# Kernel tuning notes

Hardware: AMD Instinct MI355X
Metric: run time of the kernel (lower is better)

## Reference

```python
import jax, jax.numpy as jnp
import numpy as np

B, T = 8, 1024
D = 256          # n_embd
NH = 4           # n_head
MULT = 4         # mlp_internal_dim_multiplier
GRID = 32        # grid_size, T == GRID*GRID
NLAYER = 3
N = D * MULT // NH   # sparse head dim = 256
EPS = 1e-5


def _freqs_2d(h, w, dim, theta=10000.0):
    # matches get_freqs_2d_fixed: returns (h*w, dim//2) complex64
    dim_half = dim // 2
    freqs = 1.0 / theta ** (np.arange(0, dim_half, 2, dtype=np.float32) / dim_half)
    fx = np.outer(np.arange(w, dtype=np.float32), freqs)
    fy = np.outer(np.arange(h, dtype=np.float32), freqs)
    cx = np.exp(1j * fx).astype(np.complex64)          # (w, dim_half/2)
    cy = np.exp(1j * fy).astype(np.complex64)          # (h, dim_half/2)
    gx = np.broadcast_to(cx[None, :, :], (h, w, cx.shape[-1]))
    gy = np.broadcast_to(cy[:, None, :], (h, w, cy.shape[-1]))
    return np.concatenate([gx, gy], axis=-1).reshape(h * w, -1)

FREQS = jnp.asarray(_freqs_2d(GRID, GRID, N))  # (T, N//2) complex64


def _rope(x):
    # x: (B, nh, T, N) real -> complex pairs, rotate, back to real
    xc = x.reshape(*x.shape[:-1], -1, 2)
    xc = jax.lax.complex(xc[..., 0], xc[..., 1])       # (B, nh, T, N/2)
    xr = xc * FREQS[None, None, :, :]
    out = jnp.stack([jnp.real(xr), jnp.imag(xr)], axis=-1)
    return out.reshape(x.shape).astype(x.dtype)


def _ln(x):
    # LayerNorm over last dim, no affine (biased variance, like torch)
    m = jnp.mean(x, axis=-1, keepdims=True)
    v = jnp.var(x, axis=-1, keepdims=True)
    return (x - m) / jnp.sqrt(v + EPS)


def setup_inputs() -> dict:
    key = jax.random.key(0)
    ks = jax.random.split(key, 6)
    std = 0.02
    return {
        "inputs": jax.random.normal(ks[0], (B, T), dtype=jnp.float32),
        "in_w": jax.random.normal(ks[1], (D, 1), dtype=jnp.float32) * std,
        "in_b": jnp.zeros((D,), dtype=jnp.float32),
        "encoder": jax.random.normal(ks[2], (NH, D, N), dtype=jnp.float32) * std,
        "encoder_v": jax.random.normal(ks[3], (NH, D, N), dtype=jnp.float32) * std,
        "decoder": jax.random.normal(ks[4], (NH * N, D), dtype=jnp.float32) * std,
        "out_w": jax.random.normal(ks[5], (1, D), dtype=jnp.float32) * std,
        "out_b": jnp.zeros((1,), dtype=jnp.float32),
    }


def reference(inputs, in_w, in_b, encoder, encoder_v, decoder, out_w, out_b):
    # input projection: (B,T,1) @ (1,D) + b -> (B,T,D)
    x = inputs[..., None] * in_w[None, None, :, 0].swapaxes(-1, -1)  # placeholder
    x = inputs[..., None] @ in_w.T + in_b                            # (B,T,D)
    x = _ln(x)
    scale = 1.0 / jnp.sqrt(jnp.asarray(N, dtype=x.dtype))
    for _ in range(NLAYER):
        # encoder: (B,T,D) x (nh,D,N) -> (B,nh,T,N)
        x_sparse = jax.nn.relu(jnp.einsum('btd,hdn->bhtn', x, encoder))
        QR = _rope(x_sparse)
        KR = _rope(x_sparse)
        scores = jnp.einsum('bhtn,bhsn->bhts', QR, KR) * scale       # (B,nh,T,T)
        attn = jax.nn.softmax(scores, axis=-1)
        yKV = jnp.einsum('bhts,bsd->bhtd', attn, x)                  # V = x, broadcast over heads
        yKV = _ln(yKV)
        y_sparse = jax.nn.relu(jnp.einsum('bhtd,hdn->bhtn', yKV, encoder_v))
        xy_sparse = x_sparse * y_sparse                              # (B,nh,T,N)
        # (B,nh,T,N) -> (B,T,nh*N) @ (nh*N,D) -> (B,T,D)
        yMLP = xy_sparse.transpose(0, 2, 1, 3).reshape(B, T, NH * N) @ decoder
        x = _ln(x + _ln(yMLP))
    logits = x @ out_w.T + out_b                                     # (B,T,1)
    return logits
```

## Files before the change

### kernel.cpp

```cpp
#include <hip/hip_runtime.h>
#include <hip/hip_bf16.h>
#include <math.h>

#define B_ 8
#define T_ 1024
#define D_ 256
#define NH_ 4
#define N_ 256
#define EPS_ 1e-5f

typedef __attribute__((ext_vector_type(8))) short short8_t;
typedef __attribute__((ext_vector_type(4))) float floatx4;

__device__ inline unsigned short f2bf(float f) {
    unsigned u = __builtin_bit_cast(unsigned, f);
    u += 0x7FFFu + ((u >> 16) & 1u);
    return (unsigned short)(u >> 16);
}
__device__ inline float bf2f(unsigned short h) {
    return __builtin_bit_cast(float, (unsigned)h << 16);
}

__device__ inline void gload_lds16(const unsigned short* g, unsigned short* l) {
    __builtin_amdgcn_global_load_lds(
        (const __attribute__((address_space(1))) unsigned int*)g,
        (__attribute__((address_space(3))) unsigned int*)l, 16, 0, 0);
}

__device__ inline float2 block_stats_256(float v, float* red) {
    float s1 = v, s2 = v * v;
    #pragma unroll
    for (int o = 32; o > 0; o >>= 1) { s1 += __shfl_down(s1, o); s2 += __shfl_down(s2, o); }
    int wave = threadIdx.x >> 6, lane = threadIdx.x & 63;
    __syncthreads();
    if (lane == 0) { red[wave] = s1; red[4 + wave] = s2; }
    __syncthreads();
    float S1 = red[0] + red[1] + red[2] + red[3];
    float S2 = red[4] + red[5] + red[6] + red[7];
    float mean = S1 * (1.f / 256.f);
    float var  = S2 * (1.f / 256.f) - mean * mean;
    return make_float2(mean, var);
}

__global__ __launch_bounds__(256) void k_wT(
    const float* __restrict__ in, unsigned short* __restrict__ outh,
    unsigned short* __restrict__ outl, int R, int C)
{
    __shared__ float tile[64][65];
    int c0 = blockIdx.x * 64, r0 = blockIdx.y * 64, h = blockIdx.z;
    in += (size_t)h * R * C;
    for (int i = threadIdx.x; i < 4096; i += 256) {
        int r = i >> 6, c = i & 63;
        tile[r][c] = in[(size_t)(r0 + r) * C + c0 + c];
    }
    __syncthreads();
    for (int i = threadIdx.x; i < 4096; i += 256) {
        int c = i >> 6, r = i & 63;
        float v = tile[r][c];
        unsigned short hb = f2bf(v);
        size_t o = (size_t)(h * C + c0 + c) * R + r0 + r;
        outh[o] = hb;
        outl[o] = f2bf(v - bf2f(hb));
    }
}

__global__ __launch_bounds__(256) void k_input_ln(
    const float* __restrict__ inputs, const float* __restrict__ in_w,
    const float* __restrict__ in_b, float* __restrict__ x,
    unsigned short* __restrict__ xh, unsigned short* __restrict__ xl)
{
    __shared__ float red[8];
    int row = blockIdx.x;
    int d = threadIdx.x;
    float v = inputs[row] * in_w[d] + in_b[d];
    float2 mv = block_stats_256(v, red);
    float o = (v - mv.x) * rsqrtf(mv.y + EPS_);
    size_t idx = (size_t)row * D_ + d;
    x[idx] = o;
    unsigned short hb = f2bf(o);
    xh[idx] = hb;
    xl[idx] = f2bf(o - bf2f(hb));
}

#define PG 40
template<int MODE>
__global__ __launch_bounds__(256, 2) void k_gemm_mfma(
    const unsigned short* __restrict__ Ah, const unsigned short* __restrict__ Al,
    const unsigned short* __restrict__ Wh, const unsigned short* __restrict__ Wl,
    const unsigned short* __restrict__ xsh, const unsigned short* __restrict__ xsl,
    unsigned short* __restrict__ outh, unsigned short* __restrict__ outl,
    float* __restrict__ outf,
    unsigned short* __restrict__ qrh, unsigned short* __restrict__ qrl)
{
    constexpr int K = (MODE == 2) ? 1024 : 256;
    __shared__ unsigned short As_h[128 * PG], As_l[128 * PG];
    __shared__ unsigned short Ws_h[128 * PG], Ws_l[128 * PG];
    int tid = threadIdx.x;
    int w = tid >> 6, lane = tid & 63, quad = lane >> 4, l16 = lane & 15;
    int wm = w >> 1, wn = w & 1;
    int m0 = blockIdx.y * 128, n0x = blockIdx.x * 128;
    size_t a_row0, w_row0, out_row0;
    int col0;
    int koff = 0, kend = K;
    if (MODE == 1) {
        int bh = blockIdx.z;
        a_row0 = (size_t)bh * 1024 + m0;
        w_row0 = (size_t)((bh & 3) * 256 + n0x);
        out_row0 = (size_t)(bh >> 2) * 1024 + m0;
        col0 = (bh & 3) * 256 + n0x;
    } else {
        a_row0 = m0; w_row0 = n0x; out_row0 = m0; col0 = n0x;
        if (MODE == 2) { koff = blockIdx.z * 256; kend = koff + 256; }
    }
    floatx4 acc[4][4];
    #pragma unroll
    for (int mt = 0; mt < 4; mt++)
        #pragma unroll
        for (int nt = 0; nt < 4; nt++)
            acc[mt][nt] = (floatx4){0.f, 0.f, 0.f, 0.f};

    for (int k0 = koff; k0 < kend; k0 += 32) {
        #pragma unroll
        for (int it = 0; it < 2; it++) {
            int fl = tid + it * 256;
            int row = fl >> 2, ch = fl & 3;
            size_t ga = (a_row0 + row) * (size_t)K + k0 + ch * 8;
            size_t gw = (w_row0 + row) * (size_t)K + k0 + ch * 8;
            *(short8_t*)&As_h[row * PG + ch * 8] = *(const short8_t*)(Ah + ga);
            *(short8_t*)&As_l[row * PG + ch * 8] = *(const short8_t*)(Al + ga);
            *(short8_t*)&Ws_h[row * PG + ch * 8] = *(const short8_t*)(Wh + gw);
            *(short8_t*)&Ws_l[row * PG + ch * 8] = *(const short8_t*)(Wl + gw);
        }
        __syncthreads();
        short8_t afh[4], afl[4], bfh[4], bfl[4];
        #pragma unroll
        for (int mt = 0; mt < 4; mt++) {
            afh[mt] = *(const short8_t*)&As_h[(wm * 64 + mt * 16 + l16) * PG + quad * 8];
            afl[mt] = *(const short8_t*)&As_l[(wm * 64 + mt * 16 + l16) * PG + quad * 8];
        }
        #pragma unroll
        for (int nt = 0; nt < 4; nt++) {
            bfh[nt] = *(const short8_t*)&Ws_h[(wn * 64 + nt * 16 + l16) * PG + quad * 8];
            bfl[nt] = *(const short8_t*)&Ws_l[(wn * 64 + nt * 16 + l16) * PG + quad * 8];
        }
        #pragma unroll
        for (int mt = 0; mt < 4; mt++)
            #pragma unroll
            for (int nt = 0; nt < 4; nt++) {
                acc[mt][nt] = __builtin_amdgcn_mfma_f32_16x16x32_bf16(afh[mt], bfh[nt], acc[mt][nt], 0, 0, 0);
                acc[mt][nt] = __builtin_amdgcn_mfma_f32_16x16x32_bf16(afh[mt], bfl[nt], acc[mt][nt], 0, 0, 0);
                acc[mt][nt] = __builtin_amdgcn_mfma_f32_16x16x32_bf16(afl[mt], bfh[nt], acc[mt][nt], 0, 0, 0);
            }
        __syncthreads();
    }

    #pragma unroll
    for (int mt = 0; mt < 4; mt++) {
        #pragma unroll
        for (int r = 0; r < 4; r++) {
            size_t grow = out_row0 + wm * 64 + mt * 16 + quad * 4 + r;
            #pragma unroll
            for (int nt = 0; nt < 4; nt++) {
                int gcol = col0 + wn * 64 + nt * 16 + l16;
                float v = acc[mt][nt][r];
                if (MODE == 0) {
                    v = fmaxf(v, 0.f);
                    size_t o = grow * 1024 + gcol;
                    unsigned short hb = f2bf(v);
                    outh[o] = hb;
                    outl[o] = f2bf(v - bf2f(hb));
                    float vp = __shfl_xor(v, 1);
                    int n = gcol & 255, h = gcol >> 8;
                    int t = (int)(grow & 1023), b = (int)(grow >> 10);
                    int p = n >> 1, j = p & 63;
                    int pos = (p < 64) ? (t & 31) : (t >> 5);
                    float f = __expf((float)j * -0.14391156f);
                    float ang = (float)pos * f;
                    float sn = __sinf(ang), cs = __cosf(ang);
                    float ro = (n & 1) ? (vp * sn + v * cs) : (v * cs - vp * sn);
                    size_t qo = (((size_t)b * NH_ + h) * T_ + t) * N_ + n;
                    unsigned short qb = f2bf(ro);
                    qrh[qo] = qb;
                    qrl[qo] = f2bf(ro - bf2f(qb));
                } else if (MODE == 1) {
                    float y = fmaxf(v, 0.f);
                    size_t o = grow * 1024 + gcol;
                    float xv = bf2f(xsh[o]) + bf2f(xsl[o]);
                    float p = xv * y;
                    unsigned short hb = f2bf(p);
                    outh[o] = hb;
                    outl[o] = f2bf(p - bf2f(hb));
                } else {
                    outf[(size_t)blockIdx.z * 2097152 + grow * 256 + gcol] = v;
                }
            }
        }
    }
}

__global__ __launch_bounds__(256) void k_xT(const float* __restrict__ x,
                                            unsigned short* __restrict__ Vfh,
                                            unsigned short* __restrict__ Vfl)
{
    __shared__ float tile[64][65];
    int t0 = blockIdx.x * 64, d0 = blockIdx.y * 64, b = blockIdx.z;
    const float* src = x + ((size_t)b * T_ + t0) * D_ + d0;
    for (int i = threadIdx.x; i < 1024; i += 256) {
        int r = i >> 4, c = i & 15;
        float4 v = *(const float4*)(src + (size_t)r * D_ + c * 4);
        tile[r][c * 4 + 0] = v.x;
        tile[r][c * 4 + 1] = v.y;
        tile[r][c * 4 + 2] = v.z;
        tile[r][c * 4 + 3] = v.w;
    }
    __syncthreads();
    for (int i = threadIdx.x; i < 1024; i += 256) {
        int d = i >> 4, c = i & 15;
        int tg = t0 + c * 4;
        int jj = tg >> 5, qd = (tg >> 3) & 3, i8 = tg & 7;
        int dg = d0 + d;
        int tn = dg >> 4, s16 = dg & 15;
        size_t o = (((size_t)b * 32 + jj) * 16 + tn) * 512 + (qd * 16 + s16) * 8 + i8;
        float v0 = tile[c * 4 + 0][d], v1 = tile[c * 4 + 1][d];
        float v2 = tile[c * 4 + 2][d], v3 = tile[c * 4 + 3][d];
        ushort4 oh, ol;
        oh.x = f2bf(v0); ol.x = f2bf(v0 - bf2f(oh.x));
        oh.y = f2bf(v1); ol.y = f2bf(v1 - bf2f(oh.y));
        oh.z = f2bf(v2); ol.z = f2bf(v2 - bf2f(oh.z));
        oh.w = f2bf(v3); ol.w = f2bf(v3 - bf2f(oh.w));
        *(ushort4*)(Vfh + o) = oh;
        *(ushort4*)(Vfl + o) = ol;
    }
}

#define PPW 36

__global__ __launch_bounds__(256, 1) void k_attn_mfma(
    const unsigned short* __restrict__ qr_h, const unsigned short* __restrict__ qr_l,
    const unsigned short* __restrict__ Vf_h, const unsigned short* __restrict__ Vf_l,
    unsigned short* __restrict__ ykvh, unsigned short* __restrict__ ykvl)
{
    __shared__ unsigned short K_h[2][16 * 512];
    __shared__ unsigned short K_l[2][16 * 512];
    __shared__ unsigned short V_h[2][16 * 512];
    __shared__ unsigned short V_l[2][16 * 512];
    __shared__ unsigned short P_h[4][16 * PPW];
    __shared__ unsigned short P_l[4][16 * PPW];

    int tid = threadIdx.x;
    int w = tid >> 6, lane = tid & 63, quad = lane >> 4, l16 = lane & 15;
    int gid = blockIdx.x;
    int bh = gid & 31, tile = gid >> 5, b = bh >> 2;
    int t0q = tile * 128;
    const unsigned short* qhb = qr_h + (size_t)bh * T_ * N_;
    const unsigned short* qlb = qr_l + (size_t)bh * T_ * N_;
    const unsigned short* vhb = Vf_h + (size_t)b * 32 * 16 * 512;
    const unsigned short* vlb = Vf_l + (size_t)b * 32 * 16 * 512;

    short8_t qfh[2][8], qfl[2][8];
    #pragma unroll
    for (int mt = 0; mt < 2; mt++)
        #pragma unroll
        for (int kc = 0; kc < 8; kc++) {
            size_t o = (size_t)(t0q + w * 32 + mt * 16 + l16) * N_ + kc * 32 + quad * 8;
            qfh[mt][kc] = *(const short8_t*)(qhb + o);
            qfl[mt][kc] = *(const short8_t*)(qlb + o);
        }

    floatx4 O[2][16];
    #pragma unroll
    for (int mt = 0; mt < 2; mt++)
        #pragma unroll
        for (int tn = 0; tn < 16; tn++) O[mt][tn] = (floatx4){0.f, 0.f, 0.f, 0.f};
    float lst[2][4] = {{0.f, 0.f, 0.f, 0.f}, {0.f, 0.f, 0.f, 0.f}};
    const float scale = 0.0625f;

    #pragma unroll
    for (int s = 0; s < 4; s++) {
        int slot = w * 4 + s;
        int ct = slot >> 3, kc = slot & 7;
        size_t go = (size_t)(ct * 16 + l16) * N_ + kc * 32 + quad * 8;
        gload_lds16(qhb + go, &K_h[0][slot * 512]);
        gload_lds16(qlb + go, &K_l[0][slot * 512]);
        size_t vo = ((size_t)slot << 9) + lane * 8;
        gload_lds16(vhb + vo, &V_h[0][slot * 512]);
        gload_lds16(vlb + vo, &V_l[0][slot * 512]);
    }

    for (int j = 0; j < 32; j++) {
        int buf = j & 1;
        __syncthreads();
        if (j < 31) {
            #pragma unroll
            for (int s = 0; s < 4; s++) {
                int slot = w * 4 + s;
                int ct = slot >> 3, kc = slot & 7;
                size_t go = (size_t)((j + 1) * 32 + ct * 16 + l16) * N_ + kc * 32 + quad * 8;
                gload_lds16(qhb + go, &K_h[buf ^ 1][slot * 512]);
                gload_lds16(qlb + go, &K_l[buf ^ 1][slot * 512]);
                size_t vo = ((size_t)((j + 1) * 16 + slot) << 9) + lane * 8;
                gload_lds16(vhb + vo, &V_h[buf ^ 1][slot * 512]);
                gload_lds16(vlb + vo, &V_l[buf ^ 1][slot * 512]);
            }
        }

        floatx4 sc[2][2];
        __builtin_amdgcn_s_setprio(1);
        #pragma unroll
        for (int ct = 0; ct < 2; ct++) {
            floatx4 a_hh0 = (floatx4){0.f, 0.f, 0.f, 0.f};
            floatx4 a_hl0 = (floatx4){0.f, 0.f, 0.f, 0.f};
            floatx4 a_lh0 = (floatx4){0.f, 0.f, 0.f, 0.f};
            floatx4 a_hh1 = (floatx4){0.f, 0.f, 0.f, 0.f};
            floatx4 a_hl1 = (floatx4){0.f, 0.f, 0.f, 0.f};
            floatx4 a_lh1 = (floatx4){0.f, 0.f, 0.f, 0.f};
            #pragma unroll
            for (int kc = 0; kc < 8; kc++) {
                short8_t bkh = *(const short8_t*)&K_h[buf][(ct * 8 + kc) * 512 + lane * 8];
                short8_t bkl = *(const short8_t*)&K_l[buf][(ct * 8 + kc) * 512 + lane * 8];
                a_hh0 = __builtin_amdgcn_mfma_f32_16x16x32_bf16(qfh[0][kc], bkh, a_hh0, 0, 0, 0);
                a_hh1 = __builtin_amdgcn_mfma_f32_16x16x32_bf16(qfh[1][kc], bkh, a_hh1, 0, 0, 0);
                a_hl0 = __builtin_amdgcn_mfma_f32_16x16x32_bf16(qfh[0][kc], bkl, a_hl0, 0, 0, 0);
                a_hl1 = __builtin_amdgcn_mfma_f32_16x16x32_bf16(qfh[1][kc], bkl, a_hl1, 0, 0, 0);
                a_lh0 = __builtin_amdgcn_mfma_f32_16x16x32_bf16(qfl[0][kc], bkh, a_lh0, 0, 0, 0);
                a_lh1 = __builtin_amdgcn_mfma_f32_16x16x32_bf16(qfl[1][kc], bkh, a_lh1, 0, 0, 0);
            }
            sc[0][ct] = (a_hh0 + a_hl0) + a_lh0;
            sc[1][ct] = (a_hh1 + a_hl1) + a_lh1;
        }
        __builtin_amdgcn_s_setprio(0);

        short8_t pah[2], pal[2];
        #pragma unroll
        for (int mt = 0; mt < 2; mt++) {
            #pragma unroll
            for (int r = 0; r < 4; r++) {
                float p0 = __expf(sc[mt][0][r] * scale - 8.f);
                float p1 = __expf(sc[mt][1][r] * scale - 8.f);
                lst[mt][r] += p0 + p1;
                unsigned short p0h = f2bf(p0), p1h = f2bf(p1);
                P_h[w][(quad * 4 + r) * PPW + l16]      = p0h;
                P_h[w][(quad * 4 + r) * PPW + 16 + l16] = p1h;
                P_l[w][(quad * 4 + r) * PPW + l16]      = f2bf(p0 - bf2f(p0h));
                P_l[w][(quad * 4 + r) * PPW + 16 + l16] = f2bf(p1 - bf2f(p1h));
            }
            pah[mt] = *(const short8_t*)&P_h[w][l16 * PPW + quad * 8];
            pal[mt] = *(const short8_t*)&P_l[w][l16 * PPW + quad * 8];
        }

        __builtin_amdgcn_s_setprio(1);
        #pragma unroll
        for (int tn = 0; tn < 16; tn++) {
            short8_t vbh = *(const short8_t*)&V_h[buf][tn * 512 + lane * 8];
            short8_t vbl = *(const short8_t*)&V_l[buf][tn * 512 + lane * 8];
            O[0][tn] = __builtin_amdgcn_mfma_f32_16x16x32_bf16(pah[0], vbh, O[0][tn], 0, 0, 0);
            O[1][tn] = __builtin_amdgcn_mfma_f32_16x16x32_bf16(pah[1], vbh, O[1][tn], 0, 0, 0);
            O[0][tn] = __builtin_amdgcn_mfma_f32_16x16x32_bf16(pah[0], vbl, O[0][tn], 0, 0, 0);
            O[1][tn] = __builtin_amdgcn_mfma_f32_16x16x32_bf16(pah[1], vbl, O[1][tn], 0, 0, 0);
            O[0][tn] = __builtin_amdgcn_mfma_f32_16x16x32_bf16(pal[0], vbh, O[0][tn], 0, 0, 0);
            O[1][tn] = __builtin_amdgcn_mfma_f32_16x16x32_bf16(pal[1], vbh, O[1][tn], 0, 0, 0);
        }
        __builtin_amdgcn_s_setprio(0);
    }

    #pragma unroll
    for (int mt = 0; mt < 2; mt++) {
        size_t obase = ((size_t)bh * T_ + t0q + w * 32 + mt * 16) * D_;
        #pragma unroll
        for (int r = 0; r < 4; r++) {
            float lsum = lst[mt][r];
            #pragma unroll
            for (int o = 1; o < 16; o <<= 1) lsum += __shfl_xor(lsum, o);
            float li = 1.f / lsum;
            float s1 = 0.f, s2 = 0.f;
            #pragma unroll
            for (int tn = 0; tn < 16; tn++) { float v = O[mt][tn][r]; s1 += v; s2 += v * v; }
            #pragma unroll
            for (int o = 1; o < 16; o <<= 1) { s1 += __shfl_xor(s1, o); s2 += __shfl_xor(s2, o); }
            float mean = s1 * li * (1.f / 256.f);
            float e2   = s2 * li * li * (1.f / 256.f);
            float var  = e2 - mean * mean;
            float rs = rsqrtf(var + EPS_);
            float a = li * rs, bb = mean * rs;
            int row = quad * 4 + r;
            #pragma unroll
            for (int tn = 0; tn < 16; tn++) {
                float v = O[mt][tn][r] * a - bb;
                size_t o = obase + (size_t)row * D_ + tn * 16 + l16;
                unsigned short hb = f2bf(v);
                ykvh[o] = hb;
                ykvl[o] = f2bf(v - bf2f(hb));
            }
        }
    }
}

__global__ __launch_bounds__(256) void k_resid_ln(float* __restrict__ x,
                                                  const float* __restrict__ ymlp,
                                                  unsigned short* __restrict__ xh,
                                                  unsigned short* __restrict__ xl)
{
    __shared__ float red[8];
    int row = blockIdx.x, d = threadIdx.x;
    size_t o = (size_t)row * D_ + d;
    float y = ymlp[o] + ymlp[o + 2097152] + ymlp[o + 2 * 2097152] + ymlp[o + 3 * 2097152];
    float2 mv1 = block_stats_256(y, red);
    float v = x[o] + (y - mv1.x) * rsqrtf(mv1.y + EPS_);
    float2 mv2 = block_stats_256(v, red);
    float out = (v - mv2.x) * rsqrtf(mv2.y + EPS_);
    x[o] = out;
    unsigned short hb = f2bf(out);
    xh[o] = hb;
    xl[o] = f2bf(out - bf2f(hb));
}

__global__ __launch_bounds__(256) void k_logits(
    const float* __restrict__ x, const float* __restrict__ out_w,
    const float* __restrict__ out_b, float* __restrict__ out)
{
    __shared__ float red[4];
    int row = blockIdx.x, d = threadIdx.x;
    float v = x[(size_t)row * D_ + d] * out_w[d];
    #pragma unroll
    for (int o = 32; o > 0; o >>= 1) v += __shfl_down(v, o);
    int wave = d >> 6, lane = d & 63;
    if (lane == 0) red[wave] = v;
    __syncthreads();
    if (d == 0) out[row] = red[0] + red[1] + red[2] + red[3] + out_b[0];
}

extern "C" void kernel_launch(void* const* d_in, const int* in_sizes, int n_in,
                              void* d_out, int out_size, void* d_ws, size_t ws_size,
                              hipStream_t stream)
{
    (void)in_sizes; (void)n_in; (void)out_size;
    if (ws_size < ((size_t)115 << 20)) return;

    const float* inputs    = (const float*)d_in[0];
    const float* in_w      = (const float*)d_in[1];
    const float* in_b      = (const float*)d_in[2];
    const float* encoder   = (const float*)d_in[3];
    const float* encoder_v = (const float*)d_in[4];
    const float* decoder   = (const float*)d_in[5];
    const float* out_w     = (const float*)d_in[6];
    const float* out_b     = (const float*)d_in[7];

    char* wsb = (char*)d_ws;
    float* x             = (float*)(wsb);
    unsigned short* x_h  = (unsigned short*)(wsb + ((size_t)8  << 20));
    unsigned short* x_l  = (unsigned short*)(wsb + ((size_t)12 << 20));
    unsigned short* Vf_h = x_h;
    unsigned short* Vf_l = x_l;
    unsigned short* xs_h = (unsigned short*)(wsb + ((size_t)16 << 20));
    unsigned short* xs_l = (unsigned short*)(wsb + ((size_t)32 << 20));
    float* ymlp          = (float*)(wsb + ((size_t)16 << 20));
    unsigned short* qr_h = (unsigned short*)(wsb + ((size_t)48 << 20));
    unsigned short* qr_l = (unsigned short*)(wsb + ((size_t)64 << 20));
    unsigned short* xy_h = qr_h;
    unsigned short* xy_l = qr_l;
    unsigned short* ykv_h = (unsigned short*)(wsb + ((size_t)80 << 20));
    unsigned short* ykv_l = (unsigned short*)(wsb + ((size_t)96 << 20));
    char* wbase = wsb + ((size_t)112 << 20);
    unsigned short* encT_h = (unsigned short*)(wbase);
    unsigned short* encT_l = (unsigned short*)(wbase + 0x80000);
    unsigned short* evT_h  = (unsigned short*)(wbase + 2 * 0x80000);
    unsigned short* evT_l  = (unsigned short*)(wbase + 3 * 0x80000);
    unsigned short* decT_h = (unsigned short*)(wbase + 4 * 0x80000);
    unsigned short* decT_l = (unsigned short*)(wbase + 5 * 0x80000);

    k_wT<<<dim3(4, 4, 4), 256, 0, stream>>>(encoder,   encT_h, encT_l, 256, 256);
    k_wT<<<dim3(4, 4, 4), 256, 0, stream>>>(encoder_v, evT_h,  evT_l,  256, 256);
    k_wT<<<dim3(4, 16, 1), 256, 0, stream>>>(decoder,  decT_h, decT_l, 1024, 256);

    k_input_ln<<<B_ * T_, 256, 0, stream>>>(inputs, in_w, in_b, x, x_h, x_l);
    for (int l = 0; l < 3; l++) {
        k_gemm_mfma<0><<<dim3(8, 64, 1), 256, 0, stream>>>(
            x_h, x_l, encT_h, encT_l, nullptr, nullptr, xs_h, xs_l, nullptr, qr_h, qr_l);
        k_xT<<<dim3(16, 4, 8), 256, 0, stream>>>(x, Vf_h, Vf_l);
        k_attn_mfma<<<256, 256, 0, stream>>>(qr_h, qr_l, Vf_h, Vf_l, ykv_h, ykv_l);
        k_gemm_mfma<1><<<dim3(2, 8, 32), 256, 0, stream>>>(
            ykv_h, ykv_l, evT_h, evT_l, xs_h, xs_l, xy_h, xy_l, nullptr, nullptr, nullptr);
        k_gemm_mfma<2><<<dim3(2, 64, 4), 256, 0, stream>>>(
            xy_h, xy_l, decT_h, decT_l, nullptr, nullptr, nullptr, nullptr, ymlp, nullptr, nullptr);
        k_resid_ln<<<B_ * T_, 256, 0, stream>>>(x, ymlp, x_h, x_l);
    }
    k_logits<<<B_ * T_, 256, 0, stream>>>(x, out_w, out_b, (float*)d_out);
}
```

Baseline: 827.8 us.

## Split attention key range across two warp groups with LDS reduction

The attention kernel now launches 512 threads per block: two groups of four waves each process half of the key/value sequence (16 chunks each) for the same 128 query rows. The partial outputs and row sums from the second group are then combined through shared memory before the LayerNorm epilogue. Double buffering is replaced by single-buffered per-group K/V tiles, refilled after a barrier once each phase has finished reading them. This doubles the waves per CU to hide latency and shortens the serial loop, at the cost of extra barriers, exposed load latency and a shared-memory reduction.

```diff
diff --git a/kernel.cpp b/kernel.cpp
--- a/kernel.cpp
+++ b/kernel.cpp
@@ -235,7 +235,7 @@
 
 #define PPW 36
 
-__global__ __launch_bounds__(256, 1) void k_attn_mfma(
+__global__ __launch_bounds__(512, 1) void k_attn_mfma(
     const unsigned short* __restrict__ qr_h, const unsigned short* __restrict__ qr_l,
     const unsigned short* __restrict__ Vf_h, const unsigned short* __restrict__ Vf_l,
     unsigned short* __restrict__ ykvh, unsigned short* __restrict__ ykvl)
@@ -244,11 +244,13 @@
     __shared__ unsigned short K_l[2][16 * 512];
     __shared__ unsigned short V_h[2][16 * 512];
     __shared__ unsigned short V_l[2][16 * 512];
-    __shared__ unsigned short P_h[4][16 * PPW];
-    __shared__ unsigned short P_l[4][16 * PPW];
+    __shared__ unsigned short P_h[8][16 * PPW];
+    __shared__ unsigned short P_l[8][16 * PPW];
+    __shared__ float l_scr[4][32];
 
     int tid = threadIdx.x;
     int w = tid >> 6, lane = tid & 63, quad = lane >> 4, l16 = lane & 15;
+    int tm = w >> 2, wp = w & 3;
     int gid = blockIdx.x;
     int bh = gid & 31, tile = gid >> 5, b = bh >> 2;
     int t0q = tile * 128;
@@ -262,7 +264,7 @@
     for (int mt = 0; mt < 2; mt++)
         #pragma unroll
         for (int kc = 0; kc < 8; kc++) {
-            size_t o = (size_t)(t0q + w * 32 + mt * 16 + l16) * N_ + kc * 32 + quad * 8;
+            size_t o = (size_t)(t0q + wp * 32 + mt * 16 + l16) * N_ + kc * 32 + quad * 8;
             qfh[mt][kc] = *(const short8_t*)(qhb + o);
             qfl[mt][kc] = *(const short8_t*)(qlb + o);
         }
@@ -277,33 +279,18 @@
 
     #pragma unroll
     for (int s = 0; s < 4; s++) {
-        int slot = w * 4 + s;
-        int ct = slot >> 3, kc = slot & 7;
-        size_t go = (size_t)(ct * 16 + l16) * N_ + kc * 32 + quad * 8;
-        gload_lds16(qhb + go, &K_h[0][slot * 512]);
-        gload_lds16(qlb + go, &K_l[0][slot * 512]);
-        size_t vo = ((size_t)slot << 9) + lane * 8;
-        gload_lds16(vhb + vo, &V_h[0][slot * 512]);
-        gload_lds16(vlb + vo, &V_l[0][slot * 512]);
-    }
-
-    for (int j = 0; j < 32; j++) {
-        int buf = j & 1;
-        __syncthreads();
-        if (j < 31) {
-            #pragma unroll
-            for (int s = 0; s < 4; s++) {
-                int slot = w * 4 + s;
-                int ct = slot >> 3, kc = slot & 7;
-                size_t go = (size_t)((j + 1) * 32 + ct * 16 + l16) * N_ + kc * 32 + quad * 8;
-                gload_lds16(qhb + go, &K_h[buf ^ 1][slot * 512]);
-                gload_lds16(qlb + go, &K_l[buf ^ 1][slot * 512]);
-                size_t vo = ((size_t)((j + 1) * 16 + slot) << 9) + lane * 8;
-                gload_lds16(vhb + vo, &V_h[buf ^ 1][slot * 512]);
-                gload_lds16(vlb + vo, &V_l[buf ^ 1][slot * 512]);
-            }
-        }
-
+        int s4 = wp * 4 + s;
+        int ct = s4 >> 3, kc = s4 & 7;
+        size_t go = (size_t)(tm * 512 + ct * 16 + l16) * N_ + kc * 32 + quad * 8;
+        gload_lds16(qhb + go, &K_h[tm][s4 * 512]);
+        gload_lds16(qlb + go, &K_l[tm][s4 * 512]);
+        size_t vo = ((size_t)(tm * 256 + s4) << 9) + lane * 8;
+        gload_lds16(vhb + vo, &V_h[tm][s4 * 512]);
+        gload_lds16(vlb + vo, &V_l[tm][s4 * 512]);
+    }
+    __syncthreads();
+
+    for (int j = 0; j < 16; j++) {
         floatx4 sc[2][2];
         __builtin_amdgcn_s_setprio(1);
         #pragma unroll
@@ -316,8 +303,8 @@
             floatx4 a_lh1 = (floatx4){0.f, 0.f, 0.f, 0.f};
             #pragma unroll
             for (int kc = 0; kc < 8; kc++) {
-                short8_t bkh = *(const short8_t*)&K_h[buf][(ct * 8 + kc) * 512 + lane * 8];
-                short8_t bkl = *(const short8_t*)&K_l[buf][(ct * 8 + kc) * 512 + lane * 8];
+                short8_t bkh = *(const short8_t*)&K_h[tm][(ct * 8 + kc) * 512 + lane * 8];
+                short8_t bkl = *(const short8_t*)&K_l[tm][(ct * 8 + kc) * 512 + lane * 8];
                 a_hh0 = __builtin_amdgcn_mfma_f32_16x16x32_bf16(qfh[0][kc], bkh, a_hh0, 0, 0, 0);
                 a_hh1 = __builtin_amdgcn_mfma_f32_16x16x32_bf16(qfh[1][kc], bkh, a_hh1, 0, 0, 0);
                 a_hl0 = __builtin_amdgcn_mfma_f32_16x16x32_bf16(qfh[0][kc], bkl, a_hl0, 0, 0, 0);
@@ -329,6 +316,18 @@
             sc[1][ct] = (a_hh1 + a_hl1) + a_lh1;
         }
         __builtin_amdgcn_s_setprio(0);
+
+        __syncthreads();
+        if (j < 15) {
+            #pragma unroll
+            for (int s = 0; s < 4; s++) {
+                int s4 = wp * 4 + s;
+                int ct = s4 >> 3, kc = s4 & 7;
+                size_t go = (size_t)((tm * 16 + j + 1) * 32 + ct * 16 + l16) * N_ + kc * 32 + quad * 8;
+                gload_lds16(qhb + go, &K_h[tm][s4 * 512]);
+                gload_lds16(qlb + go, &K_l[tm][s4 * 512]);
+            }
+        }
 
         short8_t pah[2], pal[2];
         #pragma unroll
@@ -351,8 +350,8 @@
         __builtin_amdgcn_s_setprio(1);
         #pragma unroll
         for (int tn = 0; tn < 16; tn++) {
-            short8_t vbh = *(const short8_t*)&V_h[buf][tn * 512 + lane * 8];
-            short8_t vbl = *(const short8_t*)&V_l[buf][tn * 512 + lane * 8];
+            short8_t vbh = *(const short8_t*)&V_h[tm][tn * 512 + lane * 8];
+            short8_t vbl = *(const short8_t*)&V_l[tm][tn * 512 + lane * 8];
             O[0][tn] = __builtin_amdgcn_mfma_f32_16x16x32_bf16(pah[0], vbh, O[0][tn], 0, 0, 0);
             O[1][tn] = __builtin_amdgcn_mfma_f32_16x16x32_bf16(pah[1], vbh, O[1][tn], 0, 0, 0);
             O[0][tn] = __builtin_amdgcn_mfma_f32_16x16x32_bf16(pah[0], vbl, O[0][tn], 0, 0, 0);
@@ -361,35 +360,71 @@
             O[1][tn] = __builtin_amdgcn_mfma_f32_16x16x32_bf16(pal[1], vbh, O[1][tn], 0, 0, 0);
         }
         __builtin_amdgcn_s_setprio(0);
-    }
-
-    #pragma unroll
-    for (int mt = 0; mt < 2; mt++) {
-        size_t obase = ((size_t)bh * T_ + t0q + w * 32 + mt * 16) * D_;
-        #pragma unroll
-        for (int r = 0; r < 4; r++) {
-            float lsum = lst[mt][r];
-            #pragma unroll
-            for (int o = 1; o < 16; o <<= 1) lsum += __shfl_xor(lsum, o);
-            float li = 1.f / lsum;
-            float s1 = 0.f, s2 = 0.f;
-            #pragma unroll
-            for (int tn = 0; tn < 16; tn++) { float v = O[mt][tn][r]; s1 += v; s2 += v * v; }
-            #pragma unroll
-            for (int o = 1; o < 16; o <<= 1) { s1 += __shfl_xor(s1, o); s2 += __shfl_xor(s2, o); }
-            float mean = s1 * li * (1.f / 256.f);
-            float e2   = s2 * li * li * (1.f / 256.f);
-            float var  = e2 - mean * mean;
-            float rs = rsqrtf(var + EPS_);
-            float a = li * rs, bb = mean * rs;
-            int row = quad * 4 + r;
-            #pragma unroll
-            for (int tn = 0; tn < 16; tn++) {
-                float v = O[mt][tn][r] * a - bb;
-                size_t o = obase + (size_t)row * D_ + tn * 16 + l16;
-                unsigned short hb = f2bf(v);
-                ykvh[o] = hb;
-                ykvl[o] = f2bf(v - bf2f(hb));
+
+        __syncthreads();
+        if (j < 15) {
+            #pragma unroll
+            for (int s = 0; s < 4; s++) {
+                int s4 = wp * 4 + s;
+                size_t vo = ((size_t)((tm * 16 + j + 1) * 16 + s4) << 9) + lane * 8;
+                gload_lds16(vhb + vo, &V_h[tm][s4 * 512]);
+                gload_lds16(vlb + vo, &V_l[tm][s4 * 512]);
+            }
+        }
+    }
+
+    float* scr = (float*)((wp == 0) ? (void*)K_h : (wp == 1) ? (void*)K_l
+                        : (wp == 2) ? (void*)V_h : (void*)V_l);
+    if (tm == 1) {
+        #pragma unroll
+        for (int mt = 0; mt < 2; mt++)
+            #pragma unroll
+            for (int r = 0; r < 4; r++) {
+                float ls = lst[mt][r];
+                #pragma unroll
+                for (int o = 1; o < 16; o <<= 1) ls += __shfl_xor(ls, o);
+                int row = mt * 16 + quad * 4 + r;
+                if (l16 == 0) l_scr[wp][row] = ls;
+                #pragma unroll
+                for (int tn = 0; tn < 16; tn++)
+                    scr[row * 256 + tn * 16 + l16] = O[mt][tn][r];
+            }
+    }
+    __syncthreads();
+
+    if (tm == 0) {
+        #pragma unroll
+        for (int mt = 0; mt < 2; mt++) {
+            size_t obase = ((size_t)bh * T_ + t0q + wp * 32 + mt * 16) * D_;
+            #pragma unroll
+            for (int r = 0; r < 4; r++) {
+                int row = quad * 4 + r;
+                #pragma unroll
+                for (int tn = 0; tn < 16; tn++)
+                    O[mt][tn][r] += scr[(mt * 16 + row) * 256 + tn * 16 + l16];
+                float lsum = lst[mt][r];
+                #pragma unroll
+                for (int o = 1; o < 16; o <<= 1) lsum += __shfl_xor(lsum, o);
+                lsum += l_scr[wp][mt * 16 + row];
+                float li = 1.f / lsum;
+                float s1 = 0.f, s2 = 0.f;
+                #pragma unroll
+                for (int tn = 0; tn < 16; tn++) { float v = O[mt][tn][r]; s1 += v; s2 += v * v; }
+                #pragma unroll
+                for (int o = 1; o < 16; o <<= 1) { s1 += __shfl_xor(s1, o); s2 += __shfl_xor(s2, o); }
+                float mean = s1 * li * (1.f / 256.f);
+                float e2   = s2 * li * li * (1.f / 256.f);
+                float var  = e2 - mean * mean;
+                float rs = rsqrtf(var + EPS_);
+                float a = li * rs, bb = mean * rs;
+                #pragma unroll
+                for (int tn = 0; tn < 16; tn++) {
+                    float v = O[mt][tn][r] * a - bb;
+                    size_t o = obase + (size_t)row * D_ + tn * 16 + l16;
+                    unsigned short hb = f2bf(v);
+                    ykvh[o] = hb;
+                    ykvl[o] = f2bf(v - bf2f(hb));
+                }
             }
         }
     }
@@ -477,7 +512,7 @@
         k_gemm_mfma<0><<<dim3(8, 64, 1), 256, 0, stream>>>(
             x_h, x_l, encT_h, encT_l, nullptr, nullptr, xs_h, xs_l, nullptr, qr_h, qr_l);
         k_xT<<<dim3(16, 4, 8), 256, 0, stream>>>(x, Vf_h, Vf_l);
-        k_attn_mfma<<<256, 256, 0, stream>>>(qr_h, qr_l, Vf_h, Vf_l, ykv_h, ykv_l);
+        k_attn_mfma<<<256, 512, 0, stream>>>(qr_h, qr_l, Vf_h, Vf_l, ykv_h, ykv_l);
         k_gemm_mfma<1><<<dim3(2, 8, 32), 256, 0, stream>>>(
             ykv_h, ykv_l, evT_h, evT_l, xs_h, xs_l, xy_h, xy_l, nullptr, nullptr, nullptr);
         k_gemm_mfma<2><<<dim3(2, 64, 4), 256, 0, stream>>>(
```

New measurement: 1.774 ms. 2.14x slower.

## Split attention work across wave pairs with 512-thread blocks

Applied to the files above, without the earlier changes.

The attention kernel now runs 8 waves per block instead of 4. Each pair of waves shares a 32-row query group, and each wave handles half of the key columns for the scores and half of the output columns for P·V. The P tile is written to shared memory by both halves, which adds a block barrier in the middle of each iteration; the K prefetch moves after that barrier while the V prefetch stays before it. Row sums and LayerNorm statistics are combined across the pair through shared-memory scratch before normalisation. The aim is more waves per CU to hide latency and fewer accumulator registers per wave, at the cost of an extra __syncthreads per key tile and duplicated Q fragment loads.

```diff
diff --git a/kernel.cpp b/kernel.cpp
--- a/kernel.cpp
+++ b/kernel.cpp
@@ -233,9 +233,9 @@
     }
 }
 
-#define PPW 36
-
-__global__ __launch_bounds__(256, 1) void k_attn_mfma(
+#define PPW2 36
+
+__global__ __launch_bounds__(512, 1) void k_attn_mfma(
     const unsigned short* __restrict__ qr_h, const unsigned short* __restrict__ qr_l,
     const unsigned short* __restrict__ Vf_h, const unsigned short* __restrict__ Vf_l,
     unsigned short* __restrict__ ykvh, unsigned short* __restrict__ ykvl)
@@ -244,11 +244,15 @@
     __shared__ unsigned short K_l[2][16 * 512];
     __shared__ unsigned short V_h[2][16 * 512];
     __shared__ unsigned short V_l[2][16 * 512];
-    __shared__ unsigned short P_h[4][16 * PPW];
-    __shared__ unsigned short P_l[4][16 * PPW];
+    __shared__ unsigned short P_h[4][32 * PPW2];
+    __shared__ unsigned short P_l[4][32 * PPW2];
+    __shared__ float l_scr[8][32];
+    __shared__ float s1_scr[8][32];
+    __shared__ float s2_scr[8][32];
 
     int tid = threadIdx.x;
     int w = tid >> 6, lane = tid & 63, quad = lane >> 4, l16 = lane & 15;
+    int rg = w >> 1, half = w & 1;
     int gid = blockIdx.x;
     int bh = gid & 31, tile = gid >> 5, b = bh >> 2;
     int t0q = tile * 128;
@@ -262,22 +266,22 @@
     for (int mt = 0; mt < 2; mt++)
         #pragma unroll
         for (int kc = 0; kc < 8; kc++) {
-            size_t o = (size_t)(t0q + w * 32 + mt * 16 + l16) * N_ + kc * 32 + quad * 8;
+            size_t o = (size_t)(t0q + rg * 32 + mt * 16 + l16) * N_ + kc * 32 + quad * 8;
             qfh[mt][kc] = *(const short8_t*)(qhb + o);
             qfl[mt][kc] = *(const short8_t*)(qlb + o);
         }
 
-    floatx4 O[2][16];
+    floatx4 O[2][8];
     #pragma unroll
     for (int mt = 0; mt < 2; mt++)
         #pragma unroll
-        for (int tn = 0; tn < 16; tn++) O[mt][tn] = (floatx4){0.f, 0.f, 0.f, 0.f};
+        for (int t = 0; t < 8; t++) O[mt][t] = (floatx4){0.f, 0.f, 0.f, 0.f};
     float lst[2][4] = {{0.f, 0.f, 0.f, 0.f}, {0.f, 0.f, 0.f, 0.f}};
     const float scale = 0.0625f;
 
     #pragma unroll
-    for (int s = 0; s < 4; s++) {
-        int slot = w * 4 + s;
+    for (int s = 0; s < 2; s++) {
+        int slot = w * 2 + s;
         int ct = slot >> 3, kc = slot & 7;
         size_t go = (size_t)(ct * 16 + l16) * N_ + kc * 32 + quad * 8;
         gload_lds16(qhb + go, &K_h[0][slot * 512]);
@@ -292,107 +296,123 @@
         __syncthreads();
         if (j < 31) {
             #pragma unroll
-            for (int s = 0; s < 4; s++) {
-                int slot = w * 4 + s;
+            for (int s = 0; s < 2; s++) {
+                int slot = w * 2 + s;
+                size_t vo = ((size_t)((j + 1) * 16 + slot) << 9) + lane * 8;
+                gload_lds16(vhb + vo, &V_h[buf ^ 1][slot * 512]);
+                gload_lds16(vlb + vo, &V_l[buf ^ 1][slot * 512]);
+            }
+        }
+
+        floatx4 a_hh0 = (floatx4){0.f, 0.f, 0.f, 0.f};
+        floatx4 a_hl0 = (floatx4){0.f, 0.f, 0.f, 0.f};
+        floatx4 a_lh0 = (floatx4){0.f, 0.f, 0.f, 0.f};
+        floatx4 a_hh1 = (floatx4){0.f, 0.f, 0.f, 0.f};
+        floatx4 a_hl1 = (floatx4){0.f, 0.f, 0.f, 0.f};
+        floatx4 a_lh1 = (floatx4){0.f, 0.f, 0.f, 0.f};
+        __builtin_amdgcn_s_setprio(1);
+        #pragma unroll
+        for (int kc = 0; kc < 8; kc++) {
+            short8_t bkh = *(const short8_t*)&K_h[buf][(half * 8 + kc) * 512 + lane * 8];
+            short8_t bkl = *(const short8_t*)&K_l[buf][(half * 8 + kc) * 512 + lane * 8];
+            a_hh0 = __builtin_amdgcn_mfma_f32_16x16x32_bf16(qfh[0][kc], bkh, a_hh0, 0, 0, 0);
+            a_hh1 = __builtin_amdgcn_mfma_f32_16x16x32_bf16(qfh[1][kc], bkh, a_hh1, 0, 0, 0);
+            a_hl0 = __builtin_amdgcn_mfma_f32_16x16x32_bf16(qfh[0][kc], bkl, a_hl0, 0, 0, 0);
+            a_hl1 = __builtin_amdgcn_mfma_f32_16x16x32_bf16(qfh[1][kc], bkl, a_hl1, 0, 0, 0);
+            a_lh0 = __builtin_amdgcn_mfma_f32_16x16x32_bf16(qfl[0][kc], bkh, a_lh0, 0, 0, 0);
+            a_lh1 = __builtin_amdgcn_mfma_f32_16x16x32_bf16(qfl[1][kc], bkh, a_lh1, 0, 0, 0);
+        }
+        __builtin_amdgcn_s_setprio(0);
+        floatx4 sc0 = (a_hh0 + a_hl0) + a_lh0;
+        floatx4 sc1 = (a_hh1 + a_hl1) + a_lh1;
+
+        #pragma unroll
+        for (int r = 0; r < 4; r++) {
+            float p0 = __expf(sc0[r] * scale - 8.f);
+            float p1 = __expf(sc1[r] * scale - 8.f);
+            lst[0][r] += p0;
+            lst[1][r] += p1;
+            int row0 = quad * 4 + r, row1 = 16 + quad * 4 + r;
+            unsigned short p0h = f2bf(p0), p1h = f2bf(p1);
+            P_h[rg][row0 * PPW2 + half * 16 + l16] = p0h;
+            P_h[rg][row1 * PPW2 + half * 16 + l16] = p1h;
+            P_l[rg][row0 * PPW2 + half * 16 + l16] = f2bf(p0 - bf2f(p0h));
+            P_l[rg][row1 * PPW2 + half * 16 + l16] = f2bf(p1 - bf2f(p1h));
+        }
+
+        __syncthreads();
+        if (j < 31) {
+            #pragma unroll
+            for (int s = 0; s < 2; s++) {
+                int slot = w * 2 + s;
                 int ct = slot >> 3, kc = slot & 7;
                 size_t go = (size_t)((j + 1) * 32 + ct * 16 + l16) * N_ + kc * 32 + quad * 8;
                 gload_lds16(qhb + go, &K_h[buf ^ 1][slot * 512]);
                 gload_lds16(qlb + go, &K_l[buf ^ 1][slot * 512]);
-                size_t vo = ((size_t)((j + 1) * 16 + slot) << 9) + lane * 8;
-                gload_lds16(vhb + vo, &V_h[buf ^ 1][slot * 512]);
-                gload_lds16(vlb + vo, &V_l[buf ^ 1][slot * 512]);
             }
         }
 
-        floatx4 sc[2][2];
+        short8_t pah0 = *(const short8_t*)&P_h[rg][(l16) * PPW2 + quad * 8];
+        short8_t pal0 = *(const short8_t*)&P_l[rg][(l16) * PPW2 + quad * 8];
+        short8_t pah1 = *(const short8_t*)&P_h[rg][(16 + l16) * PPW2 + quad * 8];
+        short8_t pal1 = *(const short8_t*)&P_l[rg][(16 + l16) * PPW2 + quad * 8];
+
         __builtin_amdgcn_s_setprio(1);
         #pragma unroll
-        for (int ct = 0; ct < 2; ct++) {
-            floatx4 a_hh0 = (floatx4){0.f, 0.f, 0.f, 0.f};
-            floatx4 a_hl0 = (floatx4){0.f, 0.f, 0.f, 0.f};
-            floatx4 a_lh0 = (floatx4){0.f, 0.f, 0.f, 0.f};
-            floatx4 a_hh1 = (floatx4){0.f, 0.f, 0.f, 0.f};
-            floatx4 a_hl1 = (floatx4){0.f, 0.f, 0.f, 0.f};
-            floatx4 a_lh1 = (floatx4){0.f, 0.f, 0.f, 0.f};
-            #pragma unroll
-            for (int kc = 0; kc < 8; kc++) {
-                short8_t bkh = *(const short8_t*)&K_h[buf][(ct * 8 + kc) * 512 + lane * 8];
-                short8_t bkl = *(const short8_t*)&K_l[buf][(ct * 8 + kc) * 512 + lane * 8];
-                a_hh0 = __builtin_amdgcn_mfma_f32_16x16x32_bf16(qfh[0][kc], bkh, a_hh0, 0, 0, 0);
-                a_hh1 = __builtin_amdgcn_mfma_f32_16x16x32_bf16(qfh[1][kc], bkh, a_hh1, 0, 0, 0);
-                a_hl0 = __builtin_amdgcn_mfma_f32_16x16x32_bf16(qfh[0][kc], bkl, a_hl0, 0, 0, 0);
-                a_hl1 = __builtin_amdgcn_mfma_f32_16x16x32_bf16(qfh[1][kc], bkl, a_hl1, 0, 0, 0);
-                a_lh0 = __builtin_amdgcn_mfma_f32_16x16x32_bf16(qfl[0][kc], bkh, a_lh0, 0, 0, 0);
-                a_lh1 = __builtin_amdgcn_mfma_f32_16x16x32_bf16(qfl[1][kc], bkh, a_lh1, 0, 0, 0);
-            }
-            sc[0][ct] = (a_hh0 + a_hl0) + a_lh0;
-            sc[1][ct] = (a_hh1 + a_hl1) + a_lh1;
-        }
-        __builtin_amdgcn_s_setprio(0);
-
-        short8_t pah[2], pal[2];
-        #pragma unroll
-        for (int mt = 0; mt < 2; mt++) {
-            #pragma unroll
-            for (int r = 0; r < 4; r++) {
-                float p0 = __expf(sc[mt][0][r] * scale - 8.f);
-                float p1 = __expf(sc[mt][1][r] * scale - 8.f);
-                lst[mt][r] += p0 + p1;
-                unsigned short p0h = f2bf(p0), p1h = f2bf(p1);
-                P_h[w][(quad * 4 + r) * PPW + l16]      = p0h;
-                P_h[w][(quad * 4 + r) * PPW + 16 + l16] = p1h;
-                P_l[w][(quad * 4 + r) * PPW + l16]      = f2bf(p0 - bf2f(p0h));
-                P_l[w][(quad * 4 + r) * PPW + 16 + l16] = f2bf(p1 - bf2f(p1h));
-            }
-            pah[mt] = *(const short8_t*)&P_h[w][l16 * PPW + quad * 8];
-            pal[mt] = *(const short8_t*)&P_l[w][l16 * PPW + quad * 8];
-        }
-
-        __builtin_amdgcn_s_setprio(1);
-        #pragma unroll
-        for (int tn = 0; tn < 16; tn++) {
+        for (int t = 0; t < 8; t++) {
+            int tn = half * 8 + t;
             short8_t vbh = *(const short8_t*)&V_h[buf][tn * 512 + lane * 8];
             short8_t vbl = *(const short8_t*)&V_l[buf][tn * 512 + lane * 8];
-            O[0][tn] = __builtin_amdgcn_mfma_f32_16x16x32_bf16(pah[0], vbh, O[0][tn], 0, 0, 0);
-            O[1][tn] = __builtin_amdgcn_mfma_f32_16x16x32_bf16(pah[1], vbh, O[1][tn], 0, 0, 0);
-            O[0][tn] = __builtin_amdgcn_mfma_f32_16x16x32_bf16(pah[0], vbl, O[0][tn], 0, 0, 0);
-            O[1][tn] = __builtin_amdgcn_mfma_f32_16x16x32_bf16(pah[1], vbl, O[1][tn], 0, 0, 0);
-            O[0][tn] = __builtin_amdgcn_mfma_f32_16x16x32_bf16(pal[0], vbh, O[0][tn], 0, 0, 0);
-            O[1][tn] = __builtin_amdgcn_mfma_f32_16x16x32_bf16(pal[1], vbh, O[1][tn], 0, 0, 0);
+            O[0][t] = __builtin_amdgcn_mfma_f32_16x16x32_bf16(pah0, vbh, O[0][t], 0, 0, 0);
+            O[1][t] = __builtin_amdgcn_mfma_f32_16x16x32_bf16(pah1, vbh, O[1][t], 0, 0, 0);
+            O[0][t] = __builtin_amdgcn_mfma_f32_16x16x32_bf16(pah0, vbl, O[0][t], 0, 0, 0);
+            O[1][t] = __builtin_amdgcn_mfma_f32_16x16x32_bf16(pah1, vbl, O[1][t], 0, 0, 0);
+            O[0][t] = __builtin_amdgcn_mfma_f32_16x16x32_bf16(pal0, vbh, O[0][t], 0, 0, 0);
+            O[1][t] = __builtin_amdgcn_mfma_f32_16x16x32_bf16(pal1, vbh, O[1][t], 0, 0, 0);
         }
         __builtin_amdgcn_s_setprio(0);
     }
 
     #pragma unroll
-    for (int mt = 0; mt < 2; mt++) {
-        size_t obase = ((size_t)bh * T_ + t0q + w * 32 + mt * 16) * D_;
+    for (int mt = 0; mt < 2; mt++)
         #pragma unroll
         for (int r = 0; r < 4; r++) {
-            float lsum = lst[mt][r];
-            #pragma unroll
-            for (int o = 1; o < 16; o <<= 1) lsum += __shfl_xor(lsum, o);
-            float li = 1.f / lsum;
+            float ls = lst[mt][r];
+            #pragma unroll
+            for (int o = 1; o < 16; o <<= 1) ls += __shfl_xor(ls, o);
             float s1 = 0.f, s2 = 0.f;
             #pragma unroll
-            for (int tn = 0; tn < 16; tn++) { float v = O[mt][tn][r]; s1 += v; s2 += v * v; }
+            for (int t = 0; t < 8; t++) { float v = O[mt][t][r]; s1 += v; s2 += v * v; }
             #pragma unroll
             for (int o = 1; o < 16; o <<= 1) { s1 += __shfl_xor(s1, o); s2 += __shfl_xor(s2, o); }
+            int row = mt * 16 + quad * 4 + r;
+            if (l16 == 0) { l_scr[w][row] = ls; s1_scr[w][row] = s1; s2_scr[w][row] = s2; }
+        }
+    __syncthreads();
+    #pragma unroll
+    for (int mt = 0; mt < 2; mt++)
+        #pragma unroll
+        for (int r = 0; r < 4; r++) {
+            int row = mt * 16 + quad * 4 + r;
+            float ls = l_scr[w][row] + l_scr[w ^ 1][row];
+            float s1 = s1_scr[w][row] + s1_scr[w ^ 1][row];
+            float s2 = s2_scr[w][row] + s2_scr[w ^ 1][row];
+            float li = 1.f / ls;
             float mean = s1 * li * (1.f / 256.f);
             float e2   = s2 * li * li * (1.f / 256.f);
             float var  = e2 - mean * mean;
             float rs = rsqrtf(var + EPS_);
             float a = li * rs, bb = mean * rs;
-            int row = quad * 4 + r;
-            #pragma unroll
-            for (int tn = 0; tn < 16; tn++) {
-                float v = O[mt][tn][r] * a - bb;
-                size_t o = obase + (size_t)row * D_ + tn * 16 + l16;
+            size_t obase = ((size_t)bh * T_ + t0q + rg * 32 + row) * D_;
+            #pragma unroll
+            for (int t = 0; t < 8; t++) {
+                float v = O[mt][t][r] * a - bb;
+                size_t o = obase + half * 128 + t * 16 + l16;
                 unsigned short hb = f2bf(v);
                 ykvh[o] = hb;
                 ykvl[o] = f2bf(v - bf2f(hb));
             }
         }
-    }
 }
 
 __global__ __launch_bounds__(256) void k_resid_ln(float* __restrict__ x,
@@ -477,7 +497,7 @@
         k_gemm_mfma<0><<<dim3(8, 64, 1), 256, 0, stream>>>(
             x_h, x_l, encT_h, encT_l, nullptr, nullptr, xs_h, xs_l, nullptr, qr_h, qr_l);
         k_xT<<<dim3(16, 4, 8), 256, 0, stream>>>(x, Vf_h, Vf_l);
-        k_attn_mfma<<<256, 256, 0, stream>>>(qr_h, qr_l, Vf_h, Vf_l, ykv_h, ykv_l);
+        k_attn_mfma<<<256, 512, 0, stream>>>(qr_h, qr_l, Vf_h, Vf_l, ykv_h, ykv_l);
         k_gemm_mfma<1><<<dim3(2, 8, 32), 256, 0, stream>>>(
             ykv_h, ykv_l, evT_h, evT_l, xs_h, xs_l, xy_h, xy_l, nullptr, nullptr, nullptr);
         k_gemm_mfma<2><<<dim3(2, 64, 4), 256, 0, stream>>>(
```

Measured after the change: 720.7 us. 12.9% less time.
